# Kernel tuning notes

Measured on AMD Instinct MI355X. Metric: run time of the kernel, lower is better.

## Reference

```python
import jax, jax.numpy as jnp
import numpy as np

B, S, E = 4, 2048, 768
DFF = 4 * E
EPS = 1e-5


def _layernorm(x, g, b):
    mu = jnp.mean(x, axis=-1, keepdims=True)
    var = jnp.mean(jnp.square(x - mu), axis=-1, keepdims=True)
    return (x - mu) * jax.lax.rsqrt(var + EPS) * g + b


def setup_inputs() -> dict:
    key = jax.random.key(0)
    ks = jax.random.split(key, 16)
    w = lambda k, shp: jax.random.normal(k, shp, dtype=jnp.float32) * 0.02
    inp = {
        "x": jax.random.normal(ks[0], (B, S, E), dtype=jnp.float32),
        "kv": jax.random.normal(ks[1], (B, S, E), dtype=jnp.float32),
        "wq_w": w(ks[2], (E, E)), "wq_b": jnp.zeros((E,), jnp.float32),
        "wk_w": w(ks[3], (E, E)), "wk_b": jnp.zeros((E,), jnp.float32),
        "wv_w": w(ks[4], (E, E)), "wv_b": jnp.zeros((E,), jnp.float32),
        "ln1_g": jnp.ones((E,), jnp.float32), "ln1_b": jnp.zeros((E,), jnp.float32),
        "wq2_w": w(ks[5], (E, E)), "wq2_b": jnp.zeros((E,), jnp.float32),
        "wk2_w": w(ks[6], (E, E)), "wk2_b": jnp.zeros((E,), jnp.float32),
        "wv2_w": w(ks[7], (E, E)), "wv2_b": jnp.zeros((E,), jnp.float32),
        "ln2_g": jnp.ones((E,), jnp.float32), "ln2_b": jnp.zeros((E,), jnp.float32),
        "w1": w(ks[8], (DFF, E)), "b1": jnp.zeros((DFF,), jnp.float32),
        "w2": w(ks[9], (E, DFF)), "b2": jnp.zeros((E,), jnp.float32),
        "ln3_g": jnp.ones((E,), jnp.float32), "ln3_b": jnp.zeros((E,), jnp.float32),
    }
    return inp


def reference(x, kv, wq_w, wq_b, wk_w, wk_b, wv_w, wv_b, ln1_g, ln1_b,
              wq2_w, wq2_b, wk2_w, wk2_b, wv2_w, wv2_b, ln2_g, ln2_b,
              w1, b1, w2, b2, ln3_g, ln3_b):
    scalar = 1.0 / np.sqrt(E).astype(np.float32)
    mask_value = jnp.finfo(x.dtype).min
    s = x.shape[1]
    causal = jnp.triu(jnp.ones((s, s), dtype=bool), k=1)  # True above diagonal -> masked

    # ---- causal self-attention (single head, full E) ----
    q = x @ wq_w.T + wq_b
    k = x @ wk_w.T + wk_b
    v = x @ wv_w.T + wv_b
    scores = jnp.einsum('bqe,bke->bqk', q, k) * scalar
    scores = jnp.where(causal, mask_value, scores)
    h1 = jnp.einsum('bqk,bke->bqe', jax.nn.softmax(scores, axis=-1), v)
    x = _layernorm(x + h1, ln1_g, ln1_b)

    # ---- cross-attention over kv (no mask) ----
    q2 = x @ wq2_w.T + wq2_b
    k2 = kv @ wk2_w.T + wk2_b
    v2 = kv @ wv2_w.T + wv2_b
    scores2 = jnp.einsum('bqe,bke->bqk', q2, k2) * scalar
    h2 = jnp.einsum('bqk,bke->bqe', jax.nn.softmax(scores2, axis=-1), v2)
    x = _layernorm(x + h2, ln2_g, ln2_b)

    # ---- MLP: Linear -> ReLU -> Linear -> ReLU (note trailing ReLU) ----
    h = jax.nn.relu(x @ w1.T + b1)
    mlp = jax.nn.relu(h @ w2.T + b2)
    return _layernorm(x + mlp, ln3_g, ln3_b)
```

## Files before the change

kernel.cpp:

```cpp
#include <hip/hip_runtime.h>
#include <hip/hip_bf16.h>
#include <math.h>


typedef __bf16 bf16_t;
typedef bf16_t bf16x8 __attribute__((ext_vector_type(8)));
typedef float f32x4 __attribute__((ext_vector_type(4)));

struct MMDesc {
    const bf16_t* A;
    const bf16_t* B;
    const float* bias;
    __hip_bfloat16* C;
    float* lsum;
    int koff;
    int trans;
};
struct MMArgs { MMDesc g[8]; };

__device__ __forceinline__ void load16(const bf16_t* g, bf16_t* l) {
    __builtin_amdgcn_global_load_lds(
        (const __attribute__((address_space(1))) unsigned int*)g,
        (__attribute__((address_space(3))) unsigned int*)l, 16, 0, 0);
}

__device__ __forceinline__ void rd4(const bf16_t* p, int s0, int s1, bf16x8 f[4][2]) {
#pragma unroll
    for (int i = 0; i < 4; ++i) {
        f[i][0] = *(const bf16x8*)(p + i * 1024 + s0);
        f[i][1] = *(const bf16x8*)(p + i * 1024 + s1);
    }
}
__device__ __forceinline__ void rd2(const bf16_t* p, int s0, int s1, bf16x8 f[2][2]) {
#pragma unroll
    for (int i = 0; i < 2; ++i) {
        f[i][0] = *(const bf16x8*)(p + i * 1024 + s0);
        f[i][1] = *(const bf16x8*)(p + i * 1024 + s1);
    }
}

#define SBAR asm volatile("s_barrier" ::: "memory")
#define SCH  __builtin_amdgcn_sched_barrier(0)
#define PBAR do { SCH; SBAR; SCH; } while (0)
#define PRIO1 __builtin_amdgcn_s_setprio(1)
#define PRIO0 __builtin_amdgcn_s_setprio(0)
#define VMC4 asm volatile("s_waitcnt vmcnt(4)" ::: "memory")

#define QMFMA(mh, nh, BF) do { \
    _Pragma("unroll") \
    for (int ks = 0; ks < 2; ++ks) \
    _Pragma("unroll") \
    for (int mi = 0; mi < 4; ++mi) \
    _Pragma("unroll") \
    for (int ni = 0; ni < 2; ++ni) \
        acc[(mh) * 4 + mi][(nh) * 2 + ni] = __builtin_amdgcn_mfma_f32_16x16x32_bf16( \
            af[mi][ks], BF[ni][ks], acc[(mh) * 4 + mi][(nh) * 2 + ni], 0, 0, 0); \
} while (0)

__device__ __forceinline__ void mm8_core(
    const bf16_t* Ag, const bf16_t* Bg, int lda, int ldb, int K,
    bf16_t* lds, int w, int l, f32x4 acc[8][4])
{
    const long ldal = lda, ldbl = ldb;
    const int fr = l & 15, kq = l >> 4;
    const int rr = w * 8 + (l >> 3);
    const int c8e = ((l & 7) ^ (l >> 3)) * 8;
    const bf16_t* As = Ag + (long)rr * ldal + c8e;
    const bf16_t* Bs = Bg + (long)rr * ldbl + c8e;
    const int s0 = ((0 + kq) ^ (fr & 7)) * 8;
    const int s1 = ((4 + kq) ^ (fr & 7)) * 8;
    const bf16_t* lA = lds + ((w >> 2) * 64 + fr) * 64;
    const bf16_t* lB = lds + 16384 + ((w & 3) * 32 + fr) * 64;
    bf16_t* stA = lds + w * 512;
    bf16_t* stB = lds + 16384 + w * 512;

    auto stg = [&](int b, int isB, int h, int t) {
        const long ld = isB ? ldbl : ldal;
        const bf16_t* g = (isB ? Bs : As) + (long)h * 128 * ld + (long)t * 64;
        bf16_t* d = (isB ? stB : stA) + b * 32768 + h * 8192;
        load16(g, d);
        load16(g + 64 * ld, d + 4096);
    };

    bf16x8 af[4][2], bf0[2][2], bf1[2][2];
    const int NT = K >> 6, NI = NT >> 1;

    stg(0, 0, 0, 0); stg(0, 1, 0, 0); stg(0, 1, 1, 0); stg(0, 0, 1, 0);
    stg(1, 0, 0, 1); stg(1, 1, 0, 1);
    asm volatile("s_waitcnt vmcnt(4)" ::: "memory");
    SBAR; SCH;

    for (int i = 0; i < NI; ++i) {
        const int t1 = 2 * i + 1;
        int t2 = 2 * i + 2; if (t2 >= NT) t2 -= 2;
        int t3 = 2 * i + 3; if (t3 >= NT) t3 -= 2;
        rd4(lA, s0, s1, af); rd2(lB, s0, s1, bf0);
        stg(1, 1, 1, t1);
        PBAR; PRIO1; QMFMA(0, 0, bf0); PRIO0;
        rd2(lB + 8192, s0, s1, bf1);
        stg(1, 0, 1, t1);
        PBAR; PRIO1; QMFMA(0, 1, bf1); PRIO0;
        rd4(lA + 8192, s0, s1, af);
        stg(0, 0, 0, t2);
        PBAR; PRIO1; QMFMA(1, 0, bf0); PRIO0;
        stg(0, 1, 0, t2);
        VMC4;
        PBAR; PRIO1; QMFMA(1, 1, bf1); PRIO0;
        rd4(lA + 32768, s0, s1, af); rd2(lB + 32768, s0, s1, bf0);
        stg(0, 1, 1, t2);
        PBAR; PRIO1; QMFMA(0, 0, bf0); PRIO0;
        rd2(lB + 32768 + 8192, s0, s1, bf1);
        stg(0, 0, 1, t2);
        PBAR; PRIO1; QMFMA(0, 1, bf1); PRIO0;
        rd4(lA + 32768 + 8192, s0, s1, af);
        stg(1, 0, 0, t3);
        PBAR; PRIO1; QMFMA(1, 0, bf0); PRIO0;
        stg(1, 1, 0, t3);
        VMC4;
        PBAR; PRIO1; QMFMA(1, 1, bf1); PRIO0;
    }
    asm volatile("s_waitcnt vmcnt(0)" ::: "memory");
    SBAR; SCH;
}

template <bool RELU, bool CLAMPK>
__global__ __launch_bounds__(512, 2) void mm8_std(
    MMArgs args, int M, int N, int K, int lda, int ldb, float scale, int GX)
{
    __shared__ __align__(16) bf16_t lds[65536];
    const MMDesc dsc = args.g[blockIdx.z];

    const int lin = blockIdx.x;
    const int panel = lin / (8 * GX);
    const int rem = lin - panel * 8 * GX;
    const int bx = rem >> 3;
    const int by = panel * 8 + (rem & 7);
    const int m0 = by * 256, n0 = bx * 256;
    const int tid = threadIdx.x, w = tid >> 6, l = tid & 63;

    f32x4 acc[8][4];
    const f32x4 z4 = {0.f, 0.f, 0.f, 0.f};
#pragma unroll
    for (int i = 0; i < 8; ++i)
#pragma unroll
        for (int j = 0; j < 4; ++j) acc[i][j] = z4;

    int Keff = K;
    if (CLAMPK) {
        int km = (by + 1) * 256 - dsc.koff;
        Keff = km < K ? km : K;
    }
    if (!CLAMPK || Keff > 0)
        mm8_core(dsc.A + (long)m0 * lda, dsc.B + (long)n0 * ldb,
                 lda, ldb, Keff, lds, w, l, acc);

    const int fr = l & 15, erow = (l >> 4) * 4;
    const int wrow = (w >> 2) * 64, wcol = (w & 3) * 32;
    __hip_bfloat16* ct = (__hip_bfloat16*)lds;
#pragma unroll
    for (int mh = 0; mh < 2; ++mh) {
        if (mh) __syncthreads();
#pragma unroll
        for (int nh = 0; nh < 2; ++nh)
#pragma unroll
            for (int ni = 0; ni < 2; ++ni) {
                const int cl = nh * 128 + wcol + ni * 16 + fr;
                const float bv = dsc.bias ? dsc.bias[n0 + cl] : 0.f;
#pragma unroll
                for (int mi = 0; mi < 4; ++mi) {
                    const int lr = wrow + mi * 16 + erow;
                    const f32x4 a = acc[mh * 4 + mi][nh * 2 + ni];
#pragma unroll
                    for (int r = 0; r < 4; ++r) {
                        float v = a[r] * scale + bv;
                        if (RELU) v = fmaxf(v, 0.f);
                        ct[dsc.trans ? (cl * 136 + lr + r) : ((lr + r) * 264 + cl)]
                            = __float2bfloat16(v);
                    }
                }
            }
        __syncthreads();
        if (dsc.trans) {
            __hip_bfloat16* base = dsc.C + ((long)(m0 >> 11) * N + n0) * 2048
                                 + (m0 & 2047) + mh * 128;
#pragma unroll
            for (int u = 0; u < 8; ++u) {
                const int e = u * 4096 + tid * 8;
                *(uint4*)(base + (long)(e >> 7) * 2048 + (e & 127))
                    = *(const uint4*)(ct + (e >> 7) * 136 + (e & 127));
            }
        } else {
            __hip_bfloat16* base = dsc.C + (long)(m0 + mh * 128) * N + n0;
#pragma unroll
            for (int u = 0; u < 8; ++u) {
                const int e = u * 4096 + tid * 8;
                *(uint4*)(base + (long)(e >> 8) * N + (e & 255))
                    = *(const uint4*)(ct + (e >> 8) * 264 + (e & 255));
            }
        }
    }
}

template <bool CAUSAL>
__global__ __launch_bounds__(512, 2) void mm8_exp(
    MMArgs args, int N, int K, int lda, int ldb, float scale, int GX)
{
    __shared__ __align__(16) bf16_t lds[65536];
    const MMDesc dsc = args.g[blockIdx.z];

    int bx, by;
    if (CAUSAL) {
        const int t = blockIdx.x;
        by = (int)((sqrtf(8.f * t + 1.f) - 1.f) * 0.5f);
        while ((by + 1) * (by + 2) / 2 <= t) ++by;
        while (by * (by + 1) / 2 > t) --by;
        bx = t - by * (by + 1) / 2;
    } else {
        const int lin = blockIdx.x;
        const int panel = lin / (8 * GX);
        const int rem = lin - panel * 8 * GX;
        bx = rem >> 3;
        by = panel * 8 + (rem & 7);
    }
    const int m0 = by * 256, n0 = bx * 256;
    const int tid = threadIdx.x, w = tid >> 6, l = tid & 63;

    f32x4 acc[8][4];
    const f32x4 z4 = {0.f, 0.f, 0.f, 0.f};
#pragma unroll
    for (int i = 0; i < 8; ++i)
#pragma unroll
        for (int j = 0; j < 4; ++j) acc[i][j] = z4;

    mm8_core(dsc.A + (long)m0 * lda, dsc.B + (long)n0 * ldb,
             lda, ldb, K, lds, w, l, acc);

    const int fr = l & 15, erow = (l >> 4) * 4;
    const int wrow = (w >> 2) * 64, wcol = (w & 3) * 32;
    __hip_bfloat16* ct = (__hip_bfloat16*)lds;
#pragma unroll
    for (int mh = 0; mh < 2; ++mh) {
        if (mh) __syncthreads();
#pragma unroll
        for (int mi = 0; mi < 4; ++mi) {
            const int lr = wrow + mi * 16 + erow;
#pragma unroll
            for (int r = 0; r < 4; ++r) {
                const int grow = m0 + mh * 128 + lr + r;
                float rs = 0.f;
#pragma unroll
                for (int nh = 0; nh < 2; ++nh)
#pragma unroll
                    for (int ni = 0; ni < 2; ++ni) {
                        const int cl = nh * 128 + wcol + ni * 16 + fr;
                        float e;
                        if (CAUSAL && (n0 + cl) > grow)
                            e = 0.f;
                        else
                            e = __expf(acc[mh * 4 + mi][nh * 2 + ni][r] * scale);
                        ct[(lr + r) * 264 + cl] = __float2bfloat16(e);
                        rs += e;
                    }
#pragma unroll
                for (int o = 8; o > 0; o >>= 1) rs += __shfl_down(rs, o, 16);
                if ((l & 15) == 0) atomicAdd(&dsc.lsum[grow], rs);
            }
        }
        __syncthreads();
        __hip_bfloat16* base = dsc.C + (long)(m0 + mh * 128) * N + n0;
#pragma unroll
        for (int u = 0; u < 8; ++u) {
            const int e = u * 4096 + tid * 8;
            *(uint4*)(base + (long)(e >> 8) * N + (e & 255))
                = *(const uint4*)(ct + (e >> 8) * 264 + (e & 255));
        }
    }
}

__device__ __forceinline__ float waveReduceSum(float v) {
#pragma unroll
    for (int o = 32; o > 0; o >>= 1) v += __shfl_down(v, o, 64);
    return v;
}
__device__ __forceinline__ float blockReduceSum(float v, float* s) {
    int lane = threadIdx.x & 63, w = threadIdx.x >> 6;
    v = waveReduceSum(v);
    __syncthreads();
    if (lane == 0) s[w] = v;
    __syncthreads();
    return s[0] + s[1] + s[2] + s[3];
}

template <bool BR, bool XF32>
__global__ __launch_bounds__(256) void ln_kernel(
    const float* __restrict__ xf, const __hip_bfloat16* __restrict__ xh,
    const __hip_bfloat16* __restrict__ h1, const __hip_bfloat16* __restrict__ h2,
    const float* __restrict__ hbias, const float* __restrict__ lsum,
    const float* __restrict__ g, const float* __restrict__ beta,
    float* __restrict__ outf, __hip_bfloat16* __restrict__ outb) {
    __shared__ float red[4];
    const int E = 768;
    const long row = blockIdx.x;
    const float hscale = lsum ? (1.f / lsum[row]) : 1.f;

    float vals[3];
    float sum = 0.f;
#pragma unroll
    for (int i = 0; i < 3; ++i) {
        int c = threadIdx.x + i * 256;
        float t = __bfloat162float(h1[row * E + c]) + __bfloat162float(h2[row * E + c]);
        if (BR) t = fmaxf(t + hbias[c], 0.f);
        else t *= hscale;
        float xv = XF32 ? xf[row * E + c] : __bfloat162float(xh[row * E + c]);
        vals[i] = xv + t;
        sum += vals[i];
    }
    sum = blockReduceSum(sum, red);
    const float mean = sum * (1.f / 768.f);

    float ss = 0.f;
#pragma unroll
    for (int i = 0; i < 3; ++i) {
        float d = vals[i] - mean;
        ss += d * d;
    }
    ss = blockReduceSum(ss, red);
    const float inv = rsqrtf(ss * (1.f / 768.f) + 1e-5f);

#pragma unroll
    for (int i = 0; i < 3; ++i) {
        int c = threadIdx.x + i * 256;
        float v = (vals[i] - mean) * inv * g[c] + beta[c];
        if (outf) outf[row * E + c] = v;
        if (outb) outb[row * E + c] = __float2bfloat16(v);
    }
}

struct CvtPtrs {
    const float* s[10];
    __hip_bfloat16* d[10];
};
__global__ __launch_bounds__(256) void cvt_all(CvtPtrs p) {
    int bid = blockIdx.x, seg, off;
    if (bid < 3456) {
        seg = bid / 576;
        off = (bid % 576) * 1024;
    } else if (bid < 8064) {
        int t = bid - 3456;
        seg = 6 + t / 2304;
        off = (t % 2304) * 1024;
    } else {
        int t = bid - 8064;
        seg = 8 + t / 6144;
        off = (t % 6144) * 1024;
    }
    const float* s = p.s[seg];
    __hip_bfloat16* d = p.d[seg];
    int i = off + threadIdx.x * 4;
    float4 v = *(const float4*)(s + i);
    d[i + 0] = __float2bfloat16(v.x);
    d[i + 1] = __float2bfloat16(v.y);
    d[i + 2] = __float2bfloat16(v.z);
    d[i + 3] = __float2bfloat16(v.w);
}

extern "C" void kernel_launch(void* const* d_in, const int* in_sizes, int n_in,
                              void* d_out, int out_size, void* d_ws, size_t ws_size,
                              hipStream_t stream) {
    const int Bb = 4, S = 2048, E = 768, DFF = 3072;
    const int Nr = Bb * S;

    const float* x    = (const float*)d_in[0];
    const float* kv   = (const float*)d_in[1];
    const float* wq_w = (const float*)d_in[2];
    const float* wq_b = (const float*)d_in[3];
    const float* wk_w = (const float*)d_in[4];
    const float* wk_b = (const float*)d_in[5];
    const float* wv_w = (const float*)d_in[6];
    const float* wv_b = (const float*)d_in[7];
    const float* ln1g = (const float*)d_in[8];
    const float* ln1b = (const float*)d_in[9];
    const float* wq2w = (const float*)d_in[10];
    const float* wq2b = (const float*)d_in[11];
    const float* wk2w = (const float*)d_in[12];
    const float* wk2b = (const float*)d_in[13];
    const float* wv2w = (const float*)d_in[14];
    const float* wv2b = (const float*)d_in[15];
    const float* ln2g = (const float*)d_in[16];
    const float* ln2b = (const float*)d_in[17];
    const float* w1   = (const float*)d_in[18];
    const float* b1   = (const float*)d_in[19];
    const float* w2   = (const float*)d_in[20];
    const float* b2   = (const float*)d_in[21];
    const float* ln3g = (const float*)d_in[22];
    const float* ln3b = (const float*)d_in[23];
    float* out = (float*)d_out;

    char* wsp = (char*)d_ws;
    auto alloc = [&](size_t bytes) {
        char* p = wsp;
        wsp += (bytes + 255) & ~(size_t)255;
        return p;
    };
    const size_t nSE = (size_t)Nr * E;
    const size_t nSS = (size_t)Bb * S * S;
    __hip_bfloat16* Pb   = (__hip_bfloat16*)alloc(nSS * 2);
    __hip_bfloat16* qb   = (__hip_bfloat16*)alloc(nSE * 2);
    __hip_bfloat16* kb   = (__hip_bfloat16*)alloc(nSE * 2);
    __hip_bfloat16* hffb = Pb;
    __hip_bfloat16* vtb  = (__hip_bfloat16*)alloc(nSE * 2);
    __hip_bfloat16* xb   = (__hip_bfloat16*)alloc(nSE * 2);
    __hip_bfloat16* kvb  = (__hip_bfloat16*)alloc(nSE * 2);
    __hip_bfloat16* actb = (__hip_bfloat16*)alloc(nSE * 2);
    __hip_bfloat16* hA   = (__hip_bfloat16*)alloc(nSE * 2);
    __hip_bfloat16* hB   = (__hip_bfloat16*)alloc(nSE * 2);
    __hip_bfloat16* wqb   = (__hip_bfloat16*)alloc((size_t)E * E * 2);
    __hip_bfloat16* wkb   = (__hip_bfloat16*)alloc((size_t)E * E * 2);
    __hip_bfloat16* wvb   = (__hip_bfloat16*)alloc((size_t)E * E * 2);
    __hip_bfloat16* wq2bm = (__hip_bfloat16*)alloc((size_t)E * E * 2);
    __hip_bfloat16* wk2bm = (__hip_bfloat16*)alloc((size_t)E * E * 2);
    __hip_bfloat16* wv2bm = (__hip_bfloat16*)alloc((size_t)E * E * 2);
    __hip_bfloat16* w1b   = (__hip_bfloat16*)alloc((size_t)DFF * E * 2);
    __hip_bfloat16* w2b   = (__hip_bfloat16*)alloc((size_t)E * DFF * 2);
    float* lsum1 = (float*)alloc((size_t)Nr * 4);
    float* lsum2 = (float*)alloc((size_t)Nr * 4);

    __hip_bfloat16* k2b  = (__hip_bfloat16*)d_out;
    __hip_bfloat16* vtb2 = k2b + nSE;

    const float scale = 1.0f / sqrtf((float)E);
    const dim3 blk(256);
    const dim3 blk5(512);

    hipMemsetAsync(lsum1, 0, (size_t)Nr * 4 * 2, stream);

    CvtPtrs cp;
    cp.s[0] = wq_w; cp.d[0] = wqb;
    cp.s[1] = wk_w; cp.d[1] = wkb;
    cp.s[2] = wv_w; cp.d[2] = wvb;
    cp.s[3] = wq2w; cp.d[3] = wq2bm;
    cp.s[4] = wk2w; cp.d[4] = wk2bm;
    cp.s[5] = wv2w; cp.d[5] = wv2bm;
    cp.s[6] = w1;   cp.d[6] = w1b;
    cp.s[7] = w2;   cp.d[7] = w2b;
    cp.s[8] = x;    cp.d[8] = xb;
    cp.s[9] = kv;   cp.d[9] = kvb;
    cvt_all<<<8064 + 12288, blk, 0, stream>>>(cp);

    {
        MMArgs a{};
        a.g[0] = {(const bf16_t*)xb,  (const bf16_t*)wqb,   wq_b, qb,   nullptr, 0, 0};
        a.g[1] = {(const bf16_t*)xb,  (const bf16_t*)wkb,   wk_b, kb,   nullptr, 0, 0};
        a.g[2] = {(const bf16_t*)xb,  (const bf16_t*)wvb,   wv_b, vtb,  nullptr, 0, 1};
        a.g[3] = {(const bf16_t*)kvb, (const bf16_t*)wk2bm, wk2b, k2b,  nullptr, 0, 0};
        a.g[4] = {(const bf16_t*)kvb, (const bf16_t*)wv2bm, wv2b, vtb2, nullptr, 0, 1};
        mm8_std<false, false><<<dim3(96, 1, 5), blk5, 0, stream>>>(
            a, Nr, E, E, E, E, 1.f, 3);
    }
    {
        MMArgs a{};
        for (int b = 0; b < 4; ++b)
            a.g[b] = {(const bf16_t*)qb + (long)b * S * E,
                      (const bf16_t*)kb + (long)b * S * E, nullptr,
                      Pb + (long)b * S * S, lsum1 + b * S, 0, 0};
        mm8_exp<true><<<dim3(36, 1, 4), blk5, 0, stream>>>(a, S, E, E, E, scale, 8);
    }
    {
        MMArgs a{};
        for (int b = 0; b < 4; ++b)
            for (int ks = 0; ks < 2; ++ks)
                a.g[b * 2 + ks] = {(const bf16_t*)Pb + (long)b * S * S + ks * 1024,
                                   (const bf16_t*)vtb + (long)b * E * S + ks * 1024,
                                   nullptr, (ks ? hB : hA) + (long)b * S * E,
                                   nullptr, ks * 1024, 0};
        mm8_std<false, true><<<dim3(24, 1, 8), blk5, 0, stream>>>(
            a, S, E, 1024, S, S, 1.f, 3);
    }
    ln_kernel<false, true><<<Nr, blk, 0, stream>>>(
        x, nullptr, hA, hB, nullptr, lsum1, ln1g, ln1b, nullptr, actb);

    {
        MMArgs a{};
        a.g[0] = {(const bf16_t*)actb, (const bf16_t*)wq2bm, wq2b, qb, nullptr, 0, 0};
        mm8_std<false, false><<<dim3(96, 1, 1), blk5, 0, stream>>>(
            a, Nr, E, E, E, E, 1.f, 3);
    }
    {
        MMArgs a{};
        for (int b = 0; b < 4; ++b)
            a.g[b] = {(const bf16_t*)qb + (long)b * S * E,
                      (const bf16_t*)k2b + (long)b * S * E, nullptr,
                      Pb + (long)b * S * S, lsum2 + b * S, 0, 0};
        mm8_exp<false><<<dim3(64, 1, 4), blk5, 0, stream>>>(a, S, E, E, E, scale, 8);
    }
    {
        MMArgs a{};
        for (int b = 0; b < 4; ++b)
            for (int ks = 0; ks < 2; ++ks)
                a.g[b * 2 + ks] = {(const bf16_t*)Pb + (long)b * S * S + ks * 1024,
                                   (const bf16_t*)vtb2 + (long)b * E * S + ks * 1024,
                                   nullptr, (ks ? hB : hA) + (long)b * S * E,
                                   nullptr, 0, 0};
        mm8_std<false, false><<<dim3(24, 1, 8), blk5, 0, stream>>>(
            a, S, E, 1024, S, S, 1.f, 3);
    }
    ln_kernel<false, false><<<Nr, blk, 0, stream>>>(
        nullptr, actb, hA, hB, nullptr, lsum2, ln2g, ln2b, nullptr, actb);

    {
        MMArgs a{};
        a.g[0] = {(const bf16_t*)actb, (const bf16_t*)w1b, b1, hffb, nullptr, 0, 0};
        mm8_std<true, false><<<dim3(384, 1, 1), blk5, 0, stream>>>(
            a, Nr, DFF, E, E, E, 1.f, 12);
    }
    {
        MMArgs a{};
        a.g[0] = {(const bf16_t*)hffb, (const bf16_t*)w2b, nullptr, hA, nullptr, 0, 0};
        a.g[1] = {(const bf16_t*)hffb + 1536, (const bf16_t*)w2b + 1536, nullptr,
                  hB, nullptr, 0, 0};
        mm8_std<false, false><<<dim3(96, 1, 2), blk5, 0, stream>>>(
            a, Nr, E, 1536, DFF, DFF, 1.f, 3);
    }
    ln_kernel<true, false><<<Nr, blk, 0, stream>>>(
        nullptr, actb, hA, hB, b2, nullptr, ln3g, ln3b, out, nullptr);
}
```

Measured before the change: 496.1 us.

## Deepen GEMM prefetch, add XCD-aware block swizzle, vectorize transposed epilogue stores

The main loop issues global-to-LDS loads one stage earlier and waits at vmcnt(6) instead of vmcnt(4), keeping more loads in flight behind the MFMAs. Block indices are remapped so that consecutive tiles land on the same XCD, which should improve L2 reuse across the eight chiplets. The transposed epilogue writes 4-wide bf16 vectors into LDS with a padded stride of 140 and reads them back as two 8-byte pieces. The risks are more outstanding memory operations, possible LDS bank conflicts at the new padding, and correctness if the reordered stage timing is wrong.

```diff
diff --git a/kernel.cpp b/kernel.cpp
--- a/kernel.cpp
+++ b/kernel.cpp
@@ -4,6 +4,7 @@
 
 
 typedef __bf16 bf16_t;
+typedef bf16_t bf16x4 __attribute__((ext_vector_type(4)));
 typedef bf16_t bf16x8 __attribute__((ext_vector_type(8)));
 typedef float f32x4 __attribute__((ext_vector_type(4)));
 
@@ -18,6 +19,13 @@
 };
 struct MMArgs { MMDesc g[8]; };
 
+__device__ __forceinline__ int xcd_swz(int bid, int nwg) {
+    const int q = nwg >> 3, r = nwg & 7;
+    const int xcd = bid & 7, o = bid >> 3;
+    const int base = (xcd < r) ? xcd * (q + 1) : r * (q + 1) + (xcd - r) * q;
+    return base + o;
+}
+
 __device__ __forceinline__ void load16(const bf16_t* g, bf16_t* l) {
     __builtin_amdgcn_global_load_lds(
         (const __attribute__((address_space(1))) unsigned int*)g,
@@ -44,7 +52,7 @@
 #define PBAR do { SCH; SBAR; SCH; } while (0)
 #define PRIO1 __builtin_amdgcn_s_setprio(1)
 #define PRIO0 __builtin_amdgcn_s_setprio(0)
-#define VMC4 asm volatile("s_waitcnt vmcnt(4)" ::: "memory")
+#define VMC6 asm volatile("s_waitcnt vmcnt(6)" ::: "memory")
 
 #define QMFMA(mh, nh, BF) do { \
     _Pragma("unroll") \
@@ -86,8 +94,8 @@
     const int NT = K >> 6, NI = NT >> 1;
 
     stg(0, 0, 0, 0); stg(0, 1, 0, 0); stg(0, 1, 1, 0); stg(0, 0, 1, 0);
-    stg(1, 0, 0, 1); stg(1, 1, 0, 1);
-    asm volatile("s_waitcnt vmcnt(4)" ::: "memory");
+    stg(1, 0, 0, 1); stg(1, 1, 0, 1); stg(1, 1, 1, 1);
+    VMC6;
     SBAR; SCH;
 
     for (int i = 0; i < NI; ++i) {
@@ -95,28 +103,26 @@
         int t2 = 2 * i + 2; if (t2 >= NT) t2 -= 2;
         int t3 = 2 * i + 3; if (t3 >= NT) t3 -= 2;
         rd4(lA, s0, s1, af); rd2(lB, s0, s1, bf0);
-        stg(1, 1, 1, t1);
+        stg(1, 0, 1, t1);
         PBAR; PRIO1; QMFMA(0, 0, bf0); PRIO0;
         rd2(lB + 8192, s0, s1, bf1);
-        stg(1, 0, 1, t1);
         PBAR; PRIO1; QMFMA(0, 1, bf1); PRIO0;
         rd4(lA + 8192, s0, s1, af);
-        stg(0, 0, 0, t2);
+        stg(0, 0, 0, t2); stg(0, 1, 0, t2);
         PBAR; PRIO1; QMFMA(1, 0, bf0); PRIO0;
-        stg(0, 1, 0, t2);
-        VMC4;
+        stg(0, 1, 1, t2);
+        VMC6;
         PBAR; PRIO1; QMFMA(1, 1, bf1); PRIO0;
         rd4(lA + 32768, s0, s1, af); rd2(lB + 32768, s0, s1, bf0);
-        stg(0, 1, 1, t2);
+        stg(0, 0, 1, t2);
         PBAR; PRIO1; QMFMA(0, 0, bf0); PRIO0;
         rd2(lB + 32768 + 8192, s0, s1, bf1);
-        stg(0, 0, 1, t2);
         PBAR; PRIO1; QMFMA(0, 1, bf1); PRIO0;
         rd4(lA + 32768 + 8192, s0, s1, af);
-        stg(1, 0, 0, t3);
+        stg(1, 0, 0, t3); stg(1, 1, 0, t3);
         PBAR; PRIO1; QMFMA(1, 0, bf0); PRIO0;
-        stg(1, 1, 0, t3);
-        VMC4;
+        stg(1, 1, 1, t3);
+        VMC6;
         PBAR; PRIO1; QMFMA(1, 1, bf1); PRIO0;
     }
     asm volatile("s_waitcnt vmcnt(0)" ::: "memory");
@@ -130,7 +136,7 @@
     __shared__ __align__(16) bf16_t lds[65536];
     const MMDesc dsc = args.g[blockIdx.z];
 
-    const int lin = blockIdx.x;
+    const int lin = xcd_swz(blockIdx.x, gridDim.x);
     const int panel = lin / (8 * GX);
     const int rem = lin - panel * 8 * GX;
     const int bx = rem >> 3;
@@ -156,6 +162,7 @@
 
     const int fr = l & 15, erow = (l >> 4) * 4;
     const int wrow = (w >> 2) * 64, wcol = (w & 3) * 32;
+    bf16_t* ctb = lds;
     __hip_bfloat16* ct = (__hip_bfloat16*)lds;
 #pragma unroll
     for (int mh = 0; mh < 2; ++mh) {
@@ -170,12 +177,22 @@
                 for (int mi = 0; mi < 4; ++mi) {
                     const int lr = wrow + mi * 16 + erow;
                     const f32x4 a = acc[mh * 4 + mi][nh * 2 + ni];
-#pragma unroll
-                    for (int r = 0; r < 4; ++r) {
-                        float v = a[r] * scale + bv;
-                        if (RELU) v = fmaxf(v, 0.f);
-                        ct[dsc.trans ? (cl * 136 + lr + r) : ((lr + r) * 264 + cl)]
-                            = __float2bfloat16(v);
+                    if (dsc.trans) {
+                        bf16x4 p;
+#pragma unroll
+                        for (int r = 0; r < 4; ++r) {
+                            float v = a[r] * scale + bv;
+                            if (RELU) v = fmaxf(v, 0.f);
+                            p[r] = (bf16_t)v;
+                        }
+                        *(bf16x4*)(ctb + cl * 140 + lr) = p;
+                    } else {
+#pragma unroll
+                        for (int r = 0; r < 4; ++r) {
+                            float v = a[r] * scale + bv;
+                            if (RELU) v = fmaxf(v, 0.f);
+                            ct[(lr + r) * 264 + cl] = __float2bfloat16(v);
+                        }
                     }
                 }
             }
@@ -186,8 +203,12 @@
 #pragma unroll
             for (int u = 0; u < 8; ++u) {
                 const int e = u * 4096 + tid * 8;
-                *(uint4*)(base + (long)(e >> 7) * 2048 + (e & 127))
-                    = *(const uint4*)(ct + (e >> 7) * 136 + (e & 127));
+                const int rl = e >> 7, cl = e & 127;
+                const bf16_t* src = ctb + rl * 140 + cl;
+                const uint2 lo = *(const uint2*)(src);
+                const uint2 hi = *(const uint2*)(src + 4);
+                const uint4 v = {lo.x, lo.y, hi.x, hi.y};
+                *(uint4*)(base + (long)rl * 2048 + cl) = v;
             }
         } else {
             __hip_bfloat16* base = dsc.C + (long)(m0 + mh * 128) * N + n0;
@@ -210,13 +231,13 @@
 
     int bx, by;
     if (CAUSAL) {
-        const int t = blockIdx.x;
+        const int t = xcd_swz(blockIdx.x, gridDim.x);
         by = (int)((sqrtf(8.f * t + 1.f) - 1.f) * 0.5f);
         while ((by + 1) * (by + 2) / 2 <= t) ++by;
         while (by * (by + 1) / 2 > t) --by;
         bx = t - by * (by + 1) / 2;
     } else {
-        const int lin = blockIdx.x;
+        const int lin = xcd_swz(blockIdx.x, gridDim.x);
         const int panel = lin / (8 * GX);
         const int rem = lin - panel * 8 * GX;
         bx = rem >> 3;
```

Result: no change. 496.8 us (+0.1%).
